# Performance work log

Hardware: AMD Instinct MI355X
Metric: run time of the kernel (lower is better)

## Reference

```python
import jax, jax.numpy as jnp
import numpy as np

B, K, L = 8, 288, 16384   # K = C*kh*kw = 32*3*3
O = 64                    # output channels


def setup_inputs() -> dict:
    key = jax.random.key(0)
    k1, k2, k3 = jax.random.split(key, 3)
    x_unf = jax.random.normal(k1, (B, K, L), dtype=jnp.float32)
    w = jax.random.normal(k2, (O, 32, 3, 3), dtype=jnp.float32)
    b = jax.random.normal(k3, (O,), dtype=jnp.float32)
    gamma = jnp.float32(0.005)
    return {"x_unf": x_unf, "w": w, "b": b, "gamma": gamma}


def reference(x_unf, w, b, gamma):
    # torch: l = x_unf.transpose(1,2)[:,:,:,None] - w.view(1,1,-1,w.size(0))
    #        l = sum(l**2, dim=2); t = exp(-gamma*l) + b
    o = w.shape[0]
    wv = jnp.reshape(w, (-1,))            # row-major flatten, same as torch .view
    wv = jnp.reshape(wv, (-1, o))         # [K, O] (memory reinterpretation, NOT transpose)
    xt = jnp.transpose(x_unf, (0, 2, 1))  # [B, L, K]
    x2 = jnp.sum(xt * xt, axis=-1, keepdims=True)       # [B, L, 1]
    w2 = jnp.sum(wv * wv, axis=0)[None, None, :]        # [1, 1, O]
    xw = jnp.einsum('blk,ko->blo', xt, wv)              # [B, L, O]
    d2 = x2 + w2 - 2.0 * xw                             # [B, L, O]
    t = jnp.exp(-gamma * d2)
    return t + b
```

## Files before the change

### kernel.cpp

```cpp
#include <hip/hip_runtime.h>

#define LDIM 16384
#define KDIM 288
#define ODIM 64
#define BDIM 8

typedef float f32x4 __attribute__((ext_vector_type(4)));

__global__ __launch_bounds__(256, 4) void gauss_fp32(
    const float* __restrict__ x, const float* __restrict__ w,
    const float* __restrict__ bias, const float* __restrict__ gammap,
    float* __restrict__ out) {
  __shared__ float xs[32 * 128];
  __shared__ float ws[32 * 64];
  __shared__ float cwb[64];

  const int t = threadIdx.x;
  const int tl = t >> 3;
  const int to = t & 7;

  const long g0 = (long)blockIdx.x * 128;
  const int bidx = (int)(g0 >> 14);
  const int l0 = (int)(g0 & (LDIM - 1));
  const float* xb = x + (long)bidx * ((long)KDIM * LDIM) + l0;

  const float gamma = gammap[0];

  const float* gpx = xb + (long)tl * LDIM + to * 16;
  const float* gpw = w + tl * 64 + to * 8;
  f32x4 xa[4], wa[2];
#pragma unroll
  for (int v = 0; v < 4; ++v) xa[v] = *(const f32x4*)(gpx + v * 4);
#pragma unroll
  for (int v = 0; v < 2; ++v) wa[v] = *(const f32x4*)(gpw + v * 4);

  {
    const int seg = t >> 6, o = t & 63;
    float s = 0.f;
#pragma unroll 8
    for (int k = seg * 72; k < seg * 72 + 72; ++k) {
      float v = w[k * 64 + o];
      s = fmaf(v, v, s);
    }
    xs[t] = s;
    __syncthreads();
    if (t < 64)
      cwb[t] = -gamma * (xs[t] + xs[t + 64] + xs[t + 128] + xs[t + 192]);
  }

  float acc[4][8];
#pragma unroll
  for (int i = 0; i < 4; ++i)
#pragma unroll
    for (int j = 0; j < 8; ++j) acc[i][j] = 0.f;
  float x2a[4] = {0.f, 0.f, 0.f, 0.f};

#pragma unroll 1
  for (int kc = 0; kc < 9; ++kc) {
    __syncthreads();
#pragma unroll
    for (int v = 0; v < 4; ++v) *(f32x4*)&xs[t * 16 + v * 4] = xa[v];
#pragma unroll
    for (int v = 0; v < 2; ++v) *(f32x4*)&ws[t * 8 + v * 4] = wa[v];
    __syncthreads();

    if (kc < 8) {
      const float* nx = gpx + (long)(kc + 1) * 32 * LDIM;
      const float* nw = gpw + (kc + 1) * 32 * 64;
#pragma unroll
      for (int v = 0; v < 4; ++v) xa[v] = *(const f32x4*)(nx + v * 4);
#pragma unroll
      for (int v = 0; v < 2; ++v) wa[v] = *(const f32x4*)(nw + v * 4);
    }

#pragma unroll 8
    for (int k = 0; k < 32; ++k) {
      f32x4 x4 = *(const f32x4*)&xs[k * 128 + tl * 4];
      f32x4 w8a = *(const f32x4*)&ws[k * 64 + to * 8];
      f32x4 w8b = *(const f32x4*)&ws[k * 64 + to * 8 + 4];
#pragma unroll
      for (int i = 0; i < 4; ++i) x2a[i] = fmaf(x4[i], x4[i], x2a[i]);
#pragma unroll
      for (int i = 0; i < 4; ++i) {
#pragma unroll
        for (int j = 0; j < 4; ++j) {
          acc[i][j] = fmaf(x4[i], w8a[j], acc[i][j]);
          acc[i][j + 4] = fmaf(x4[i], w8b[j], acc[i][j + 4]);
        }
      }
    }
  }

  const float coef = 2.f * gamma;
  const f32x4 cwv_a = *(const f32x4*)&cwb[to * 8];
  const f32x4 cwv_b = *(const f32x4*)&cwb[to * 8 + 4];
  const f32x4 bv_a = *(const f32x4*)&bias[to * 8];
  const f32x4 bv_b = *(const f32x4*)&bias[to * 8 + 4];

  float* outw = out + (g0 + tl * 4) * 64 + to * 8;
#pragma unroll
  for (int i = 0; i < 4; ++i) {
    const float cx = -gamma * x2a[i];
    f32x4 r0, r1;
#pragma unroll
    for (int j = 0; j < 4; ++j) {
      r0[j] = __expf(fmaf(coef, acc[i][j], cx + cwv_a[j])) + bv_a[j];
      r1[j] = __expf(fmaf(coef, acc[i][j + 4], cx + cwv_b[j])) + bv_b[j];
    }
    *(f32x4*)(outw + i * 64) = r0;
    *(f32x4*)(outw + i * 64 + 4) = r1;
  }
}

extern "C" void kernel_launch(void* const* d_in, const int* in_sizes, int n_in,
                              void* d_out, int out_size, void* d_ws, size_t ws_size,
                              hipStream_t stream) {
  const float* x = (const float*)d_in[0];
  const float* w = (const float*)d_in[1];
  const float* b = (const float*)d_in[2];
  const float* gamma = (const float*)d_in[3];
  float* out = (float*)d_out;

  (void)d_ws; (void)ws_size;
  gauss_fp32<<<1024, 256, 0, stream>>>(x, w, b, gamma, out);
}
```

Baseline: 251.0 us.

## Double-buffer LDS with direct global-to-LDS loads and enlarge tile to 256 rows

Replaces the register-staged global loads and LDS stores with global_load_lds, which copies straight into LDS, and double-buffers the x and w tiles so the next chunk loads while the current one is computed. Each block now covers 256 L positions with an 8x8 register tile per thread, up from 4x8, and half as many blocks are launched. Bias and the |w|^2 terms are kept in registers. More registers and 80KB of LDS per block reduce occupancy (launch bounds lowered to 2), and 512 blocks may underfill the GPU's CUs.

New measurement: 241.8 us. -3.7%, faster.

```diff
diff --git a/kernel.cpp b/kernel.cpp
--- a/kernel.cpp
+++ b/kernel.cpp
@@ -7,33 +7,54 @@
 
 typedef float f32x4 __attribute__((ext_vector_type(4)));
 
-__global__ __launch_bounds__(256, 4) void gauss_fp32(
+__global__ __launch_bounds__(256, 2) void gauss_fp32(
     const float* __restrict__ x, const float* __restrict__ w,
     const float* __restrict__ bias, const float* __restrict__ gammap,
     float* __restrict__ out) {
-  __shared__ float xs[32 * 128];
-  __shared__ float ws[32 * 64];
-  __shared__ float cwb[64];
+  __shared__ float lds[2 * 8192 + 2 * 2048];
+  float* const xs0 = lds;
+  float* const ws0 = lds + 16384;
+  float* const red = ws0 + 2048;
 
   const int t = threadIdx.x;
+  const int lane = t & 63;
+  const int wvid = t >> 6;
   const int tl = t >> 3;
   const int to = t & 7;
 
-  const long g0 = (long)blockIdx.x * 128;
+  const long g0 = (long)blockIdx.x * 256;
   const int bidx = (int)(g0 >> 14);
   const int l0 = (int)(g0 & (LDIM - 1));
   const float* xb = x + (long)bidx * ((long)KDIM * LDIM) + l0;
 
+#define STAGE(KC, BUF)                                                         \
+  {                                                                            \
+    const float* xsrc = xb + (long)((KC) * 32) * LDIM + lane * 4;              \
+    float* xdst = xs0 + (BUF) * 8192;                                          \
+    _Pragma("unroll") for (int i = 0; i < 8; ++i) {                            \
+      int r = wvid * 8 + i;                                                    \
+      __builtin_amdgcn_global_load_lds(                                        \
+          (const __attribute__((address_space(1))) unsigned int*)(void*)       \
+              (xsrc + (long)r * LDIM),                                         \
+          (__attribute__((address_space(3))) unsigned int*)(void*)             \
+              (xdst + r * 256),                                                \
+          16, 0, 0);                                                           \
+    }                                                                          \
+    const float* wsrc = w + (KC) * 2048 + lane * 4;                            \
+    float* wdst = ws0 + (BUF) * 2048;                                          \
+    _Pragma("unroll") for (int j = 0; j < 2; ++j) {                            \
+      int s = wvid * 2 + j;                                                    \
+      __builtin_amdgcn_global_load_lds(                                        \
+          (const __attribute__((address_space(1))) unsigned int*)(void*)       \
+              (wsrc + s * 256),                                                \
+          (__attribute__((address_space(3))) unsigned int*)(void*)             \
+              (wdst + s * 256),                                                \
+          16, 0, 0);                                                           \
+    }                                                                          \
+  }
+
+  STAGE(0, 0)
   const float gamma = gammap[0];
-
-  const float* gpx = xb + (long)tl * LDIM + to * 16;
-  const float* gpw = w + tl * 64 + to * 8;
-  f32x4 xa[4], wa[2];
-#pragma unroll
-  for (int v = 0; v < 4; ++v) xa[v] = *(const f32x4*)(gpx + v * 4);
-#pragma unroll
-  for (int v = 0; v < 2; ++v) wa[v] = *(const f32x4*)(gpw + v * 4);
-
   {
     const int seg = t >> 6, o = t & 63;
     float s = 0.f;
@@ -42,74 +63,70 @@
       float v = w[k * 64 + o];
       s = fmaf(v, v, s);
     }
-    xs[t] = s;
-    __syncthreads();
-    if (t < 64)
-      cwb[t] = -gamma * (xs[t] + xs[t + 64] + xs[t + 128] + xs[t + 192]);
+    red[t] = s;
   }
+  __syncthreads();
 
-  float acc[4][8];
+  float cwv[8], bv[8];
 #pragma unroll
-  for (int i = 0; i < 4; ++i)
+  for (int j = 0; j < 8; ++j) {
+    int o = to * 8 + j;
+    cwv[j] = -gamma * (red[o] + red[o + 64] + red[o + 128] + red[o + 192]);
+    bv[j] = bias[o];
+  }
+  __syncthreads();
+  STAGE(1, 1)
+
+  float acc[8][8];
+#pragma unroll
+  for (int i = 0; i < 8; ++i)
 #pragma unroll
     for (int j = 0; j < 8; ++j) acc[i][j] = 0.f;
-  float x2a[4] = {0.f, 0.f, 0.f, 0.f};
+  float x2a[8] = {0.f, 0.f, 0.f, 0.f, 0.f, 0.f, 0.f, 0.f};
 
 #pragma unroll 1
   for (int kc = 0; kc < 9; ++kc) {
-    __syncthreads();
+    const float* xp = xs0 + (kc & 1) * 8192;
+    const float* wp = ws0 + (kc & 1) * 2048;
+#pragma unroll 4
+    for (int k = 0; k < 32; ++k) {
+      f32x4 xa0 = *(const f32x4*)(xp + k * 256 + tl * 8);
+      f32x4 xa1 = *(const f32x4*)(xp + k * 256 + tl * 8 + 4);
+      f32x4 wa0 = *(const f32x4*)(wp + k * 64 + to * 8);
+      f32x4 wa1 = *(const f32x4*)(wp + k * 64 + to * 8 + 4);
+      float xv[8];
 #pragma unroll
-    for (int v = 0; v < 4; ++v) *(f32x4*)&xs[t * 16 + v * 4] = xa[v];
+      for (int i = 0; i < 4; ++i) { xv[i] = xa0[i]; xv[i + 4] = xa1[i]; }
 #pragma unroll
-    for (int v = 0; v < 2; ++v) *(f32x4*)&ws[t * 8 + v * 4] = wa[v];
-    __syncthreads();
-
-    if (kc < 8) {
-      const float* nx = gpx + (long)(kc + 1) * 32 * LDIM;
-      const float* nw = gpw + (kc + 1) * 32 * 64;
+      for (int i = 0; i < 8; ++i) x2a[i] = fmaf(xv[i], xv[i], x2a[i]);
 #pragma unroll
-      for (int v = 0; v < 4; ++v) xa[v] = *(const f32x4*)(nx + v * 4);
-#pragma unroll
-      for (int v = 0; v < 2; ++v) wa[v] = *(const f32x4*)(nw + v * 4);
-    }
-
-#pragma unroll 8
-    for (int k = 0; k < 32; ++k) {
-      f32x4 x4 = *(const f32x4*)&xs[k * 128 + tl * 4];
-      f32x4 w8a = *(const f32x4*)&ws[k * 64 + to * 8];
-      f32x4 w8b = *(const f32x4*)&ws[k * 64 + to * 8 + 4];
-#pragma unroll
-      for (int i = 0; i < 4; ++i) x2a[i] = fmaf(x4[i], x4[i], x2a[i]);
-#pragma unroll
-      for (int i = 0; i < 4; ++i) {
+      for (int i = 0; i < 8; ++i) {
 #pragma unroll
         for (int j = 0; j < 4; ++j) {
-          acc[i][j] = fmaf(x4[i], w8a[j], acc[i][j]);
-          acc[i][j + 4] = fmaf(x4[i], w8b[j], acc[i][j + 4]);
+          acc[i][j] = fmaf(xv[i], wa0[j], acc[i][j]);
+          acc[i][j + 4] = fmaf(xv[i], wa1[j], acc[i][j + 4]);
         }
       }
     }
+    __syncthreads();
+    if (kc < 7) STAGE(kc + 2, kc & 1)
   }
 
   const float coef = 2.f * gamma;
-  const f32x4 cwv_a = *(const f32x4*)&cwb[to * 8];
-  const f32x4 cwv_b = *(const f32x4*)&cwb[to * 8 + 4];
-  const f32x4 bv_a = *(const f32x4*)&bias[to * 8];
-  const f32x4 bv_b = *(const f32x4*)&bias[to * 8 + 4];
-
-  float* outw = out + (g0 + tl * 4) * 64 + to * 8;
+  float* outw = out + (g0 + (long)tl * 8) * 64 + to * 8;
 #pragma unroll
-  for (int i = 0; i < 4; ++i) {
+  for (int i = 0; i < 8; ++i) {
     const float cx = -gamma * x2a[i];
     f32x4 r0, r1;
 #pragma unroll
     for (int j = 0; j < 4; ++j) {
-      r0[j] = __expf(fmaf(coef, acc[i][j], cx + cwv_a[j])) + bv_a[j];
-      r1[j] = __expf(fmaf(coef, acc[i][j + 4], cx + cwv_b[j])) + bv_b[j];
+      r0[j] = __expf(fmaf(coef, acc[i][j], cx + cwv[j])) + bv[j];
+      r1[j] = __expf(fmaf(coef, acc[i][j + 4], cx + cwv[j + 4])) + bv[j + 4];
     }
     *(f32x4*)(outw + i * 64) = r0;
     *(f32x4*)(outw + i * 64 + 4) = r1;
   }
+#undef STAGE
 }
 
 extern "C" void kernel_launch(void* const* d_in, const int* in_sizes, int n_in,
@@ -122,5 +139,5 @@
   float* out = (float*)d_out;
 
   (void)d_ws; (void)ws_size;
-  gauss_fp32<<<1024, 256, 0, stream>>>(x, w, b, gamma, out);
+  gauss_fp32<<<512, 256, 0, stream>>>(x, w, b, gamma, out);
 }
```

## Use bf16 MFMA for distance GEMM with prepacked weight fragments

Applied to the files above, without the earlier changes.

Replaces the fp32 FMA outer-product loop with bf16 16x16x32 MFMA instructions, converting x to bf16 in registers and loading it directly from global memory without LDS staging. A small pre-kernel packs the weights into MFMA B-fragment layout in workspace and computes the weight-norm term. This removes shared-memory traffic and barriers and moves the matmul onto the matrix cores. The cost is a second launch and bf16 rounding of the x·w term, which gets multiplied by 2*gamma before the exp. Stores become scalar and strided, which may weaken write coalescing.

Result: faster. 232.6 us (-7.3%).

```diff
diff --git a/kernel.cpp b/kernel.cpp
--- a/kernel.cpp
+++ b/kernel.cpp
@@ -6,109 +6,155 @@
 #define BDIM 8
 
 typedef float f32x4 __attribute__((ext_vector_type(4)));
+typedef short bf16x8 __attribute__((ext_vector_type(8)));
 
-__global__ __launch_bounds__(256, 4) void gauss_fp32(
-    const float* __restrict__ x, const float* __restrict__ w,
-    const float* __restrict__ bias, const float* __restrict__ gammap,
-    float* __restrict__ out) {
-  __shared__ float xs[32 * 128];
-  __shared__ float ws[32 * 64];
-  __shared__ float cwb[64];
+__device__ __forceinline__ short f2bf(float f) {
+  unsigned u = __builtin_bit_cast(unsigned, f);
+  unsigned r = u + 0x7FFFu + ((u >> 16) & 1u);
+  return (short)(r >> 16);
+}
 
-  const int t = threadIdx.x;
-  const int tl = t >> 3;
-  const int to = t & 7;
+__global__ __launch_bounds__(256) void gauss_pre(const float* __restrict__ w,
+                                                 const float* __restrict__ gammap,
+                                                 short* __restrict__ wfrag,
+                                                 float* __restrict__ cw) {
+  int tid = threadIdx.x;
+  int blk = blockIdx.x;
 
-  const long g0 = (long)blockIdx.x * 128;
-  const int bidx = (int)(g0 >> 14);
-  const int l0 = (int)(g0 & (LDIM - 1));
-  const float* xb = x + (long)bidx * ((long)KDIM * LDIM) + l0;
-
-  const float gamma = gammap[0];
-
-  const float* gpx = xb + (long)tl * LDIM + to * 16;
-  const float* gpw = w + tl * 64 + to * 8;
-  f32x4 xa[4], wa[2];
+  if (blk < 9) {
+    int kc = blk;
+    int ln = tid & 63;
+    int nt = tid >> 6;
+    int k0 = kc * 32 + (ln >> 4) * 8;
+    int n = nt * 16 + (ln & 15);
+    bf16x8 v;
 #pragma unroll
-  for (int v = 0; v < 4; ++v) xa[v] = *(const f32x4*)(gpx + v * 4);
-#pragma unroll
-  for (int v = 0; v < 2; ++v) wa[v] = *(const f32x4*)(gpw + v * 4);
-
-  {
-    const int seg = t >> 6, o = t & 63;
+    for (int j = 0; j < 8; ++j) v[j] = f2bf(w[(k0 + j) * 64 + n]);
+    *(bf16x8*)(wfrag + ((kc * 4 + nt) * 64 + ln) * 8) = v;
+  } else {
+    __shared__ float red[256];
+    int o = tid & 63;
+    int seg = tid >> 6;
     float s = 0.f;
 #pragma unroll 8
     for (int k = seg * 72; k < seg * 72 + 72; ++k) {
       float v = w[k * 64 + o];
       s = fmaf(v, v, s);
     }
-    xs[t] = s;
+    red[tid] = s;
     __syncthreads();
-    if (t < 64)
-      cwb[t] = -gamma * (xs[t] + xs[t + 64] + xs[t + 128] + xs[t + 192]);
+    if (tid < 64) {
+      float t = red[tid] + red[tid + 64] + red[tid + 128] + red[tid + 192];
+      cw[tid] = -gammap[0] * t;
+    }
+  }
+}
+
+__global__ __launch_bounds__(256, 4) void gauss_main(
+    const float* __restrict__ x, const short* __restrict__ wfrag,
+    const float* __restrict__ cw, const float* __restrict__ bias,
+    const float* __restrict__ gammap, float* __restrict__ out) {
+  const int t = threadIdx.x;
+  const int lane = t & 63;
+  const int wvid = t >> 6;
+  const int m = lane & 15;
+  const int g = lane >> 4;
+
+  const long g0 = (long)blockIdx.x * 128;
+  const int bidx = (int)(g0 >> 14);
+  const int l0 = (int)(g0 & (LDIM - 1));
+
+  const float* xc = x + (long)bidx * ((long)KDIM * LDIM) +
+                    (long)(g * 8) * LDIM + (l0 + wvid * 32 + m);
+
+  float xv0[8], xv1[8], nx0[8], nx1[8];
+#pragma unroll
+  for (int j = 0; j < 8; ++j) {
+    xv0[j] = xc[(long)j * LDIM];
+    xv1[j] = xc[(long)j * LDIM + 16];
   }
 
-  float acc[4][8];
+  const f32x4 zero = {0.f, 0.f, 0.f, 0.f};
+  f32x4 acc[2][4];
 #pragma unroll
-  for (int i = 0; i < 4; ++i)
+  for (int tt = 0; tt < 2; ++tt)
 #pragma unroll
-    for (int j = 0; j < 8; ++j) acc[i][j] = 0.f;
-  float x2a[4] = {0.f, 0.f, 0.f, 0.f};
+    for (int nt = 0; nt < 4; ++nt) acc[tt][nt] = zero;
+  float x2a[2] = {0.f, 0.f};
 
 #pragma unroll 1
   for (int kc = 0; kc < 9; ++kc) {
-    __syncthreads();
+    if (kc < 8) {
+      const float* nxp = xc + (long)((kc + 1) * 32) * LDIM;
 #pragma unroll
-    for (int v = 0; v < 4; ++v) *(f32x4*)&xs[t * 16 + v * 4] = xa[v];
+      for (int j = 0; j < 8; ++j) {
+        nx0[j] = nxp[(long)j * LDIM];
+        nx1[j] = nxp[(long)j * LDIM + 16];
+      }
+    }
+
+    const short* wp = wfrag + ((kc * 4) * 64 + lane) * 8;
+    bf16x8 bfr[4];
 #pragma unroll
-    for (int v = 0; v < 2; ++v) *(f32x4*)&ws[t * 8 + v * 4] = wa[v];
-    __syncthreads();
+    for (int nt = 0; nt < 4; ++nt) bfr[nt] = *(const bf16x8*)(wp + nt * 512);
+
+    bf16x8 a0, a1;
+#pragma unroll
+    for (int j = 0; j < 8; ++j) {
+      x2a[0] = fmaf(xv0[j], xv0[j], x2a[0]);
+      a0[j] = f2bf(xv0[j]);
+    }
+#pragma unroll
+    for (int j = 0; j < 8; ++j) {
+      x2a[1] = fmaf(xv1[j], xv1[j], x2a[1]);
+      a1[j] = f2bf(xv1[j]);
+    }
+
+#pragma unroll
+    for (int nt = 0; nt < 4; ++nt) {
+      acc[0][nt] = __builtin_amdgcn_mfma_f32_16x16x32_bf16(a0, bfr[nt], acc[0][nt], 0, 0, 0);
+      acc[1][nt] = __builtin_amdgcn_mfma_f32_16x16x32_bf16(a1, bfr[nt], acc[1][nt], 0, 0, 0);
+    }
 
     if (kc < 8) {
-      const float* nx = gpx + (long)(kc + 1) * 32 * LDIM;
-      const float* nw = gpw + (kc + 1) * 32 * 64;
 #pragma unroll
-      for (int v = 0; v < 4; ++v) xa[v] = *(const f32x4*)(nx + v * 4);
-#pragma unroll
-      for (int v = 0; v < 2; ++v) wa[v] = *(const f32x4*)(nw + v * 4);
-    }
-
-#pragma unroll 8
-    for (int k = 0; k < 32; ++k) {
-      f32x4 x4 = *(const f32x4*)&xs[k * 128 + tl * 4];
-      f32x4 w8a = *(const f32x4*)&ws[k * 64 + to * 8];
-      f32x4 w8b = *(const f32x4*)&ws[k * 64 + to * 8 + 4];
-#pragma unroll
-      for (int i = 0; i < 4; ++i) x2a[i] = fmaf(x4[i], x4[i], x2a[i]);
-#pragma unroll
-      for (int i = 0; i < 4; ++i) {
-#pragma unroll
-        for (int j = 0; j < 4; ++j) {
-          acc[i][j] = fmaf(x4[i], w8a[j], acc[i][j]);
-          acc[i][j + 4] = fmaf(x4[i], w8b[j], acc[i][j + 4]);
-        }
+      for (int j = 0; j < 8; ++j) {
+        xv0[j] = nx0[j];
+        xv1[j] = nx1[j];
       }
     }
   }
 
+#pragma unroll
+  for (int tt = 0; tt < 2; ++tt) {
+    x2a[tt] += __shfl_xor(x2a[tt], 16, 64);
+    x2a[tt] += __shfl_xor(x2a[tt], 32, 64);
+  }
+
+  const float gamma = gammap[0];
   const float coef = 2.f * gamma;
-  const f32x4 cwv_a = *(const f32x4*)&cwb[to * 8];
-  const f32x4 cwv_b = *(const f32x4*)&cwb[to * 8 + 4];
-  const f32x4 bv_a = *(const f32x4*)&bias[to * 8];
-  const f32x4 bv_b = *(const f32x4*)&bias[to * 8 + 4];
+  float cwv[4], bv[4];
+#pragma unroll
+  for (int nt = 0; nt < 4; ++nt) {
+    cwv[nt] = cw[nt * 16 + m];
+    bv[nt] = bias[nt * 16 + m];
+  }
 
-  float* outw = out + (g0 + tl * 4) * 64 + to * 8;
+  float* ob = out + (g0 + wvid * 32) * 64;
 #pragma unroll
-  for (int i = 0; i < 4; ++i) {
-    const float cx = -gamma * x2a[i];
-    f32x4 r0, r1;
+  for (int tt = 0; tt < 2; ++tt) {
 #pragma unroll
-    for (int j = 0; j < 4; ++j) {
-      r0[j] = __expf(fmaf(coef, acc[i][j], cx + cwv_a[j])) + bv_a[j];
-      r1[j] = __expf(fmaf(coef, acc[i][j + 4], cx + cwv_b[j])) + bv_b[j];
+    for (int r = 0; r < 4; ++r) {
+      int row = g * 4 + r;
+      float x2v = __shfl(x2a[tt], (lane & 48) | row, 64);
+      float cx = -gamma * x2v;
+      int lrow = tt * 16 + row;
+#pragma unroll
+      for (int nt = 0; nt < 4; ++nt) {
+        float e = fmaf(coef, acc[tt][nt][r], cx + cwv[nt]);
+        ob[lrow * 64 + nt * 16 + m] = __expf(e) + bv[nt];
+      }
     }
-    *(f32x4*)(outw + i * 64) = r0;
-    *(f32x4*)(outw + i * 64 + 4) = r1;
   }
 }
 
@@ -121,6 +167,9 @@
   const float* gamma = (const float*)d_in[3];
   float* out = (float*)d_out;
 
-  (void)d_ws; (void)ws_size;
-  gauss_fp32<<<1024, 256, 0, stream>>>(x, w, b, gamma, out);
+  short* wfrag = (short*)d_ws;
+  float* cw = (float*)((char*)d_ws + 36864);
+
+  gauss_pre<<<10, 256, 0, stream>>>(w, gamma, wfrag, cw);
+  gauss_main<<<1024, 256, 0, stream>>>(x, wfrag, cw, b, gamma, out);
 }
```
